# Optimization experiments

Measured on AMD Instinct MI355X. Metric: run time of the kernel, lower is better.

The kernel has to match this reference:

```python
import jax, jax.numpy as jnp
import numpy as np

N_ENVS = 8
MIN_SIGMA = 0.01

def setup_inputs() -> dict:
    key = jax.random.key(0)
    ks = jax.random.split(key, 16)
    B, T, d, L, H = 32, 64, 128, 64, 256
    H2 = H // 2
    s = 0.05
    return {
        "z_signal": jax.random.normal(ks[0], (B, T, d, L), dtype=jnp.float32),
        "z_corrupt": jax.random.normal(ks[1], (B, T, d, L), dtype=jnp.float32),
        "A": jax.random.uniform(ks[2], (d, d), dtype=jnp.float32),
        "regime": jax.random.randint(ks[3], (B,), 0, N_ENVS),
        # signal_proj: Linear(L -> H)
        "W_sig": jax.random.normal(ks[4], (L, H), dtype=jnp.float32) * s,
        "b_sig": jnp.zeros((H,), dtype=jnp.float32),
        # per-env mechanisms: Linear(H->H), ReLU, Linear(H->2), stacked over envs
        "W1e": jax.random.normal(ks[5], (N_ENVS, H, H), dtype=jnp.float32) * s,
        "b1e": jnp.zeros((N_ENVS, H), dtype=jnp.float32),
        "W2e": jax.random.normal(ks[6], (N_ENVS, H, 2), dtype=jnp.float32) * s,
        "b2e": jnp.zeros((N_ENVS, 2), dtype=jnp.float32),
        # corrupt path: Linear(L -> H//2), ReLU, Linear(H//2 -> 1)
        "Wc": jax.random.normal(ks[7], (L, H2), dtype=jnp.float32) * s,
        "bc": jnp.zeros((H2,), dtype=jnp.float32),
        "Wo": jax.random.normal(ks[8], (H2, 1), dtype=jnp.float32) * s,
        "bo": jnp.zeros((1,), dtype=jnp.float32),
    }

def reference(z_signal, z_corrupt, A, regime, W_sig, b_sig, W1e, b1e, W2e, b2e, Wc, bc, Wo, bo):
    # z_signal: [B,T,d,L], A: [d,d]
    # z_agg[b,t,i,l] = sum_j A[j,i] * z_signal[b,t,j,l]  (A^T @ z per slice)
    z_agg = jnp.einsum('ji,btjl->btil', A, z_signal)
    h_signal = jnp.einsum('btdl,lh->btdh', z_agg, W_sig) + b_sig  # [B,T,d,H]

    # env dispatch: e_idx = regime if regime < n_envs else 0 (per batch element)
    eidx = jnp.where(regime >= N_ENVS, 0, regime)
    W1 = W1e[eidx]  # [B,H,H]
    b1 = b1e[eidx]  # [B,H]
    W2 = W2e[eidx]  # [B,H,2]
    b2 = b2e[eidx]  # [B,2]

    h1 = jax.nn.relu(jnp.einsum('btdh,bhk->btdk', h_signal, W1) + b1[:, None, None, :])
    out = jnp.einsum('btdh,bhk->btdk', h1, W2) + b2[:, None, None, :]  # [B,T,d,2]
    mu = out[..., 0]
    sigma = jax.nn.softplus(out[..., 1]) + MIN_SIGMA

    # corrupt contribution
    h_c = jnp.einsum('btdl,lh->btdh', z_corrupt, Wc) + bc
    contrib = (jnp.einsum('btdh,ho->btdo', jax.nn.relu(h_c), Wo) + bo)[..., 0]  # [B,T,d]
    mu = mu + contrib
    return mu, sigma
```

## Files before the change

### kernel.cpp

```cpp
#include <hip/hip_runtime.h>
#include <hip/hip_bf16.h>


typedef __attribute__((ext_vector_type(8))) short short8;
typedef __attribute__((ext_vector_type(4))) float f32x4;

#define MFMA16(a, b, c) __builtin_amdgcn_mfma_f32_16x16x32_bf16((a), (b), (c), 0, 0, 0)

__device__ __forceinline__ unsigned short f2bf(float f) {
  union { float f; unsigned u; } v; v.f = f;
  unsigned r = v.u + 0x7fffu + ((v.u >> 16) & 1u);
  return (unsigned short)(r >> 16);
}

__device__ __forceinline__ unsigned pkbf(float a, float b) {
  __hip_bfloat162 t = __float22bfloat162_rn(float2{a, b});
  unsigned u; __builtin_memcpy(&u, &t, 4); return u;
}

union S8 { short8 s; unsigned u[4]; };

__device__ __forceinline__ void gload16(const void* gsrc, void* ldsdst) {
  __builtin_amdgcn_global_load_lds(
      (const __attribute__((address_space(1))) unsigned int*)gsrc,
      (__attribute__((address_space(3))) unsigned int*)ldsdst, 16, 0, 0);
}

__global__ void setup_k(const float* __restrict__ A, const float* __restrict__ W_sig,
                        const float* __restrict__ b_sig, const float* __restrict__ W1e,
                        const float* __restrict__ b1e, const float* __restrict__ W2e,
                        const float* __restrict__ Wc,
                        unsigned short* __restrict__ wsw1f, unsigned short* __restrict__ at_f,
                        unsigned short* __restrict__ wct_f, float* __restrict__ bw) {
  int blk = blockIdx.x, tid = threadIdx.x;
  if (blk < 512) {
    int e = blk >> 6, l = blk & 63, h = tid;
    const float* w1 = W1e + e * 65536 + h;
    const float* ws = W_sig + l * 256;
    float acc = 0.f;
    #pragma unroll 8
    for (int h1 = 0; h1 < 256; ++h1) acc = fmaf(ws[h1], w1[h1 * 256], acc);
    int c = h >> 7, ht = (h >> 4) & 7, col = h & 15;
    int kks = l >> 5, lgl = (l >> 3) & 3, e8 = l & 7;
    int lane = lgl * 16 + col;
    wsw1f[((((e * 2 + c) * 8 + ht) * 2 + kks) * 64 + lane) * 8 + e8] = f2bf(acc);
  } else if (blk < 576) {
    int idx = (blk - 512) * 256 + tid;
    int frag = idx >> 3, e8 = idx & 7;
    int it = frag >> 8, ks = (frag >> 6) & 3, lane = frag & 63;
    int j = ks * 32 + (lane >> 4) * 8 + e8, i = it * 16 + (lane & 15);
    at_f[idx] = f2bf(A[j * 128 + i]);
  } else if (blk < 608) {
    int idx = (blk - 576) * 256 + tid;
    int frag = idx >> 3, e8 = idx & 7;
    int ht = frag >> 7, ks = (frag >> 6) & 1, lane = frag & 63;
    int l = ks * 32 + (lane >> 4) * 8 + e8, h = ht * 16 + (lane & 15);
    wct_f[idx] = f2bf(Wc[l * 128 + h]);
  } else if (blk < 624) {
    int idx = (blk - 608) * 256 + tid;
    int e = idx >> 9, r = idx & 511;
    bw[e * 768 + 256 + r] = W2e[idx];
  } else {
    int e = blk - 624, h = tid;
    const float* w1 = W1e + e * 65536 + h;
    float acc = b1e[e * 256 + h];
    for (int h1 = 0; h1 < 256; ++h1) acc = fmaf(b_sig[h1], w1[h1 * 256], acc);
    bw[e * 768 + h] = acc;
  }
}

__global__ __launch_bounds__(256, 4) void dec_k(
    const float* __restrict__ zs, const float* __restrict__ zcr,
    const int* __restrict__ regime, const float* __restrict__ b2e,
    const float* __restrict__ bc, const float* __restrict__ Wo,
    const float* __restrict__ bo,
    const unsigned short* __restrict__ wsw1f, const unsigned short* __restrict__ at_f,
    const unsigned short* __restrict__ wct_f, const float* __restrict__ bw,
    float* __restrict__ out) {
  __shared__ __align__(16) char sm[35840];
  float* s_bias1 = (float*)(sm + 32768);
  float* s_W2    = s_bias1 + 256;

  const int bt = ((blockIdx.x & 7) << 8) | (blockIdx.x >> 3);
  const int tid = threadIdx.x;
  const int lane = tid & 63, wave = tid >> 6, lg = lane >> 4, l15 = lane & 15;
  int e = regime[bt >> 6]; if (e >= 8) e = 0;
  const float b2_0 = b2e[2 * e], b2_1 = b2e[2 * e + 1], bo0 = bo[0];

  const float* Z  = zs  + (size_t)bt * 8192;
  const float* Zc = zcr + (size_t)bt * 8192;

  if (wave < 3)
    gload16((const char*)(bw + e * 768) + tid * 16, sm + 32768 + wave * 1024);

  float4 z0v[4], z1v[4];
  #pragma unroll
  for (int k = 0; k < 4; ++k) {
    int g = k * 256 + tid, j = (g >> 4) * 2, l0 = (g & 15) * 4;
    const float* p = Z + j * 64 + l0;
    z0v[k] = *(const float4*)p;
    z1v[k] = *(const float4*)(p + 64);
  }
  float4 zq[2][2][2];
  #pragma unroll
  for (int q = 0; q < 2; ++q) {
    int dcol = (wave * 2 + q) * 16 + l15;
    #pragma unroll
    for (int ks = 0; ks < 2; ++ks) {
      const float* p = Zc + dcol * 64 + ks * 32 + lg * 8;
      zq[q][ks][0] = *(const float4*)p;
      zq[q][ks][1] = *(const float4*)(p + 4);
    }
  }
  #pragma unroll
  for (int k = 0; k < 4; ++k) {
    int g = k * 256 + tid, j = (g >> 4) * 2, l0 = (g & 15) * 4;
    float a0[4] = {z0v[k].x, z0v[k].y, z0v[k].z, z0v[k].w};
    float a1[4] = {z1v[k].x, z1v[k].y, z1v[k].z, z1v[k].w};
    #pragma unroll
    for (int i2 = 0; i2 < 4; ++i2) {
      int l = l0 + i2;
      unsigned v = pkbf(a0[i2], a1[i2]);
      int a = (l * 256 + j * 2) ^ ((((l >> 2) ^ l) & 7) << 4);
      *(unsigned*)(sm + a) = v;
    }
  }
  __syncthreads();

  short8 bq[2][2];
  #pragma unroll
  for (int q = 0; q < 2; ++q)
    #pragma unroll
    for (int ks = 0; ks < 2; ++ks) {
      S8 t;
      t.u[0] = pkbf(zq[q][ks][0].x, zq[q][ks][0].y);
      t.u[1] = pkbf(zq[q][ks][0].z, zq[q][ks][0].w);
      t.u[2] = pkbf(zq[q][ks][1].x, zq[q][ks][1].y);
      t.u[3] = pkbf(zq[q][ks][1].z, zq[q][ks][1].w);
      bq[q][ks] = t.s;
    }

  short8 abfr[2][4];
  #pragma unroll
  for (int m = 0; m < 2; ++m)
    #pragma unroll
    for (int ks = 0; ks < 4; ++ks)
      abfr[m][ks] = *(const short8*)(at_f + ((((wave * 2 + m) * 4 + ks) * 64 + lane) << 3));

  float cp[2] = {0.f, 0.f};
  #pragma unroll
  for (int ht = 0; ht < 8; ++ht) {
    short8 wa0 = *(const short8*)(wct_f + (((ht * 2 + 0) * 64 + lane) << 3));
    short8 wa1 = *(const short8*)(wct_f + (((ht * 2 + 1) * 64 + lane) << 3));
    float4 bcv = *(const float4*)(bc + ht * 16 + lg * 4);
    float4 wov = *(const float4*)(Wo + ht * 16 + lg * 4);
    #pragma unroll
    for (int q = 0; q < 2; ++q) {
      f32x4 acc = (f32x4){0.f, 0.f, 0.f, 0.f};
      acc = MFMA16(wa0, bq[q][0], acc);
      acc = MFMA16(wa1, bq[q][1], acc);
      #pragma unroll
      for (int r = 0; r < 4; ++r)
        cp[q] += fmaxf(acc[r] + bcv[r], 0.f) * wov[r];
    }
  }
  #pragma unroll
  for (int q = 0; q < 2; ++q) {
    cp[q] += __shfl_xor(cp[q], 16);
    cp[q] += __shfl_xor(cp[q], 32);
  }

  const unsigned short* wse = wsw1f + (size_t)e * 16384;
  short8 wsf0[8][2];
  #pragma unroll
  for (int ht = 0; ht < 8; ++ht)
    #pragma unroll
    for (int ks = 0; ks < 2; ++ks)
      wsf0[ht][ks] = *(const short8*)(wse + (((ht * 2 + ks) * 64 + lane) << 3));

  f32x4 acc1[4][2];
  #pragma unroll
  for (int lt = 0; lt < 4; ++lt)
    #pragma unroll
    for (int m = 0; m < 2; ++m) acc1[lt][m] = (f32x4){0.f, 0.f, 0.f, 0.f};
  #pragma unroll
  for (int ks = 0; ks < 4; ++ks) {
    #pragma unroll
    for (int lt = 0; lt < 4; ++lt) {
      int arow = lt * 16 + l15;
      short8 afr = *(const short8*)(sm + ((arow * 256 + lg * 16 + ks * 64) ^
                                          ((((arow >> 2) ^ arow) & 7) << 4)));
      #pragma unroll
      for (int m = 0; m < 2; ++m) acc1[lt][m] = MFMA16(afr, abfr[m][ks], acc1[lt][m]);
    }
  }
  __syncthreads();

  short8 wsf1[8][2];
  #pragma unroll
  for (int ht = 0; ht < 8; ++ht)
    #pragma unroll
    for (int ks = 0; ks < 2; ++ks)
      wsf1[ht][ks] = *(const short8*)(wse + 8192 + (((ht * 2 + ks) * 64 + lane) << 3));

  #pragma unroll
  for (int lt = 0; lt < 4; ++lt) {
    int l0 = lt * 16 + lg * 4;
    #pragma unroll
    for (int m = 0; m < 2; ++m) {
      int i = (wave * 2 + m) * 16 + l15;
      unsigned lo = pkbf(acc1[lt][m][0], acc1[lt][m][1]);
      unsigned hi = pkbf(acc1[lt][m][2], acc1[lt][m][3]);
      int a = (i * 128 + l0 * 2) ^ ((i & 7) << 4);
      *(unsigned long long*)(sm + 16384 + a) = ((unsigned long long)hi << 32) | lo;
    }
  }
  short8 mbfr[2][2];
  #pragma unroll
  for (int m = 0; m < 2; ++m) {
    int brow = (wave * 2 + m) * 16 + l15;
    #pragma unroll
    for (int ks = 0; ks < 2; ++ks)
      mbfr[m][ks] = *(const short8*)(sm + 16384 +
                       ((brow * 128 + lg * 16 + ks * 64) ^ ((brow & 7) << 4)));
  }

  float v0[2] = {0.f, 0.f}, v1[2] = {0.f, 0.f};
  #pragma unroll
  for (int c = 0; c < 2; ++c) {
    #pragma unroll
    for (int ht = 0; ht < 8; ++ht) {
      int h4 = c * 128 + ht * 16 + lg * 4;
      float4 b1v = *(const float4*)(s_bias1 + h4);
      float4 w2a = *(const float4*)(s_W2 + h4 * 2);
      float4 w2b = *(const float4*)(s_W2 + h4 * 2 + 4);
      #pragma unroll
      for (int m = 0; m < 2; ++m) {
        f32x4 acc = (f32x4){0.f, 0.f, 0.f, 0.f};
        if (c == 0) {
          acc = MFMA16(wsf0[ht][0], mbfr[m][0], acc);
          acc = MFMA16(wsf0[ht][1], mbfr[m][1], acc);
        } else {
          acc = MFMA16(wsf1[ht][0], mbfr[m][0], acc);
          acc = MFMA16(wsf1[ht][1], mbfr[m][1], acc);
        }
        float p0 = fmaxf(acc[0] + b1v.x, 0.f), p1 = fmaxf(acc[1] + b1v.y, 0.f);
        float p2 = fmaxf(acc[2] + b1v.z, 0.f), p3 = fmaxf(acc[3] + b1v.w, 0.f);
        v0[m] = fmaf(p0, w2a.x, fmaf(p1, w2a.z, fmaf(p2, w2b.x, fmaf(p3, w2b.z, v0[m]))));
        v1[m] = fmaf(p0, w2a.y, fmaf(p1, w2a.w, fmaf(p2, w2b.y, fmaf(p3, w2b.w, v1[m]))));
      }
    }
  }
  #pragma unroll
  for (int m = 0; m < 2; ++m) {
    v0[m] += __shfl_xor(v0[m], 16); v0[m] += __shfl_xor(v0[m], 32);
    v1[m] += __shfl_xor(v1[m], 16); v1[m] += __shfl_xor(v1[m], 32);
  }

  if (lane < 16) {
    #pragma unroll
    for (int m = 0; m < 2; ++m) {
      int d = (wave * 2 + m) * 16 + lane;
      float mu = v0[m] + b2_0 + bo0 + cp[m];
      float x = v1[m] + b2_1;
      float sg = fmaxf(x, 0.f) + log1pf(expf(-fabsf(x))) + 0.01f;
      out[(size_t)bt * 128 + d] = mu;
      out[262144 + (size_t)bt * 128 + d] = sg;
    }
  }
}

extern "C" void kernel_launch(void* const* d_in, const int* in_sizes, int n_in,
                              void* d_out, int out_size, void* d_ws, size_t ws_size,
                              hipStream_t stream) {
  const float* zs    = (const float*)d_in[0];
  const float* zcr   = (const float*)d_in[1];
  const float* A     = (const float*)d_in[2];
  const int*   reg   = (const int*)d_in[3];
  const float* W_sig = (const float*)d_in[4];
  const float* b_sig = (const float*)d_in[5];
  const float* W1e   = (const float*)d_in[6];
  const float* b1e   = (const float*)d_in[7];
  const float* W2e   = (const float*)d_in[8];
  const float* b2e   = (const float*)d_in[9];
  const float* Wc    = (const float*)d_in[10];
  const float* bcp   = (const float*)d_in[11];
  const float* Wo    = (const float*)d_in[12];
  const float* bo    = (const float*)d_in[13];

  unsigned short* wsw1f = (unsigned short*)d_ws;
  unsigned short* at_f  = wsw1f + 131072;
  unsigned short* wct_f = at_f + 16384;
  float* bw             = (float*)(wct_f + 8192);

  setup_k<<<632, 256, 0, stream>>>(A, W_sig, b_sig, W1e, b1e, W2e, Wc,
                                   wsw1f, at_f, wct_f, bw);
  dec_k<<<2048, 256, 0, stream>>>(zs, zcr, reg, b2e, bcp, Wo, bo,
                                  wsw1f, at_f, wct_f, bw, (float*)d_out);
}
```

Baseline: 52.45 us.

## Process two (b,t) slices per workgroup to reuse weight fragments

Each workgroup now handles two consecutive bt slices instead of one, halving the grid to 1024 blocks. Weight fragments (Wc, W_sig·W1, A) are loaded once into registers and applied to both slices, reducing global/L2 weight traffic per output. In exchange there is more register pressure, an extra barrier, and fewer workgroups for latency hiding. Both slices share the same regime index since bt0 and bt0+1 fall within the same batch.

Measured after the change: 56.51 us. +7.8%, slower.

```diff
diff --git a/kernel.cpp b/kernel.cpp
--- a/kernel.cpp
+++ b/kernel.cpp
@@ -81,63 +81,104 @@
   float* s_bias1 = (float*)(sm + 32768);
   float* s_W2    = s_bias1 + 256;
 
-  const int bt = ((blockIdx.x & 7) << 8) | (blockIdx.x >> 3);
+  const int wg = ((blockIdx.x & 7) << 7) | (blockIdx.x >> 3);
+  const int bt0 = wg * 2;
   const int tid = threadIdx.x;
   const int lane = tid & 63, wave = tid >> 6, lg = lane >> 4, l15 = lane & 15;
-  int e = regime[bt >> 6]; if (e >= 8) e = 0;
+  int e = regime[bt0 >> 6]; if (e >= 8) e = 0;
   const float b2_0 = b2e[2 * e], b2_1 = b2e[2 * e + 1], bo0 = bo[0];
-
-  const float* Z  = zs  + (size_t)bt * 8192;
-  const float* Zc = zcr + (size_t)bt * 8192;
 
   if (wave < 3)
     gload16((const char*)(bw + e * 768) + tid * 16, sm + 32768 + wave * 1024);
 
-  float4 z0v[4], z1v[4];
-  #pragma unroll
-  for (int k = 0; k < 4; ++k) {
-    int g = k * 256 + tid, j = (g >> 4) * 2, l0 = (g & 15) * 4;
-    const float* p = Z + j * 64 + l0;
-    z0v[k] = *(const float4*)p;
-    z1v[k] = *(const float4*)(p + 64);
-  }
-  float4 zq[2][2][2];
-  #pragma unroll
-  for (int q = 0; q < 2; ++q) {
-    int dcol = (wave * 2 + q) * 16 + l15;
-    #pragma unroll
-    for (int ks = 0; ks < 2; ++ks) {
-      const float* p = Zc + dcol * 64 + ks * 32 + lg * 8;
-      zq[q][ks][0] = *(const float4*)p;
-      zq[q][ks][1] = *(const float4*)(p + 4);
-    }
-  }
-  #pragma unroll
-  for (int k = 0; k < 4; ++k) {
-    int g = k * 256 + tid, j = (g >> 4) * 2, l0 = (g & 15) * 4;
-    float a0[4] = {z0v[k].x, z0v[k].y, z0v[k].z, z0v[k].w};
-    float a1[4] = {z1v[k].x, z1v[k].y, z1v[k].z, z1v[k].w};
-    #pragma unroll
-    for (int i2 = 0; i2 < 4; ++i2) {
-      int l = l0 + i2;
-      unsigned v = pkbf(a0[i2], a1[i2]);
-      int a = (l * 256 + j * 2) ^ ((((l >> 2) ^ l) & 7) << 4);
-      *(unsigned*)(sm + a) = v;
+  #pragma unroll
+  for (int g = 0; g < 2; ++g) {
+    const float* Zg = zs + (size_t)(bt0 + g) * 8192;
+    float4 z0v[4], z1v[4];
+    #pragma unroll
+    for (int k = 0; k < 4; ++k) {
+      int gg = k * 256 + tid, j = (gg >> 4) * 2, l0 = (gg & 15) * 4;
+      const float* p = Zg + j * 64 + l0;
+      z0v[k] = *(const float4*)p;
+      z1v[k] = *(const float4*)(p + 64);
+    }
+    #pragma unroll
+    for (int k = 0; k < 4; ++k) {
+      int gg = k * 256 + tid, j = (gg >> 4) * 2, l0 = (gg & 15) * 4;
+      float a0[4] = {z0v[k].x, z0v[k].y, z0v[k].z, z0v[k].w};
+      float a1[4] = {z1v[k].x, z1v[k].y, z1v[k].z, z1v[k].w};
+      #pragma unroll
+      for (int i2 = 0; i2 < 4; ++i2) {
+        int l = l0 + i2;
+        unsigned v = pkbf(a0[i2], a1[i2]);
+        int a = (l * 256 + j * 2) ^ ((((l >> 2) ^ l) & 7) << 4);
+        *(unsigned*)(sm + g * 16384 + a) = v;
+      }
     }
   }
   __syncthreads();
 
-  short8 bq[2][2];
-  #pragma unroll
-  for (int q = 0; q < 2; ++q)
-    #pragma unroll
-    for (int ks = 0; ks < 2; ++ks) {
-      S8 t;
-      t.u[0] = pkbf(zq[q][ks][0].x, zq[q][ks][0].y);
-      t.u[1] = pkbf(zq[q][ks][0].z, zq[q][ks][0].w);
-      t.u[2] = pkbf(zq[q][ks][1].x, zq[q][ks][1].y);
-      t.u[3] = pkbf(zq[q][ks][1].z, zq[q][ks][1].w);
-      bq[q][ks] = t.s;
+  short8 bq[2][2][2];
+  #pragma unroll
+  for (int g = 0; g < 2; ++g) {
+    const float* Zcg = zcr + (size_t)(bt0 + g) * 8192;
+    float4 zq[2][2][2];
+    #pragma unroll
+    for (int q = 0; q < 2; ++q) {
+      int dcol = (wave * 2 + q) * 16 + l15;
+      #pragma unroll
+      for (int ks = 0; ks < 2; ++ks) {
+        const float* p = Zcg + dcol * 64 + ks * 32 + lg * 8;
+        zq[q][ks][0] = *(const float4*)p;
+        zq[q][ks][1] = *(const float4*)(p + 4);
+      }
+    }
+    #pragma unroll
+    for (int q = 0; q < 2; ++q)
+      #pragma unroll
+      for (int ks = 0; ks < 2; ++ks) {
+        S8 t;
+        t.u[0] = pkbf(zq[q][ks][0].x, zq[q][ks][0].y);
+        t.u[1] = pkbf(zq[q][ks][0].z, zq[q][ks][0].w);
+        t.u[2] = pkbf(zq[q][ks][1].x, zq[q][ks][1].y);
+        t.u[3] = pkbf(zq[q][ks][1].z, zq[q][ks][1].w);
+        bq[g][q][ks] = t.s;
+      }
+  }
+
+  float cp[2][2] = {{0.f, 0.f}, {0.f, 0.f}};
+  #pragma unroll
+  for (int hb = 0; hb < 2; ++hb) {
+    short8 wcf[4][2];
+    #pragma unroll
+    for (int hh = 0; hh < 4; ++hh)
+      #pragma unroll
+      for (int ks = 0; ks < 2; ++ks)
+        wcf[hh][ks] = *(const short8*)(wct_f + ((((hb * 4 + hh) * 2 + ks) * 64 + lane) << 3));
+    #pragma unroll
+    for (int hh = 0; hh < 4; ++hh) {
+      int ht = hb * 4 + hh;
+      float4 bcv = *(const float4*)(bc + ht * 16 + lg * 4);
+      float4 wov = *(const float4*)(Wo + ht * 16 + lg * 4);
+      #pragma unroll
+      for (int g = 0; g < 2; ++g)
+        #pragma unroll
+        for (int q = 0; q < 2; ++q) {
+          f32x4 acc = (f32x4){0.f, 0.f, 0.f, 0.f};
+          acc = MFMA16(wcf[hh][0], bq[g][q][0], acc);
+          acc = MFMA16(wcf[hh][1], bq[g][q][1], acc);
+          #pragma unroll
+          for (int r = 0; r < 4; ++r)
+            cp[g][q] += fmaxf(acc[r] + bcv[r], 0.f) * wov[r];
+        }
+    }
+  }
+  #pragma unroll
+  for (int g = 0; g < 2; ++g)
+    #pragma unroll
+    for (int q = 0; q < 2; ++q) {
+      cp[g][q] += __shfl_xor(cp[g][q], 16);
+      cp[g][q] += __shfl_xor(cp[g][q], 32);
     }
 
   short8 abfr[2][4];
@@ -147,126 +188,109 @@
     for (int ks = 0; ks < 4; ++ks)
       abfr[m][ks] = *(const short8*)(at_f + ((((wave * 2 + m) * 4 + ks) * 64 + lane) << 3));
 
-  float cp[2] = {0.f, 0.f};
-  #pragma unroll
-  for (int ht = 0; ht < 8; ++ht) {
-    short8 wa0 = *(const short8*)(wct_f + (((ht * 2 + 0) * 64 + lane) << 3));
-    short8 wa1 = *(const short8*)(wct_f + (((ht * 2 + 1) * 64 + lane) << 3));
-    float4 bcv = *(const float4*)(bc + ht * 16 + lg * 4);
-    float4 wov = *(const float4*)(Wo + ht * 16 + lg * 4);
-    #pragma unroll
-    for (int q = 0; q < 2; ++q) {
-      f32x4 acc = (f32x4){0.f, 0.f, 0.f, 0.f};
-      acc = MFMA16(wa0, bq[q][0], acc);
-      acc = MFMA16(wa1, bq[q][1], acc);
-      #pragma unroll
-      for (int r = 0; r < 4; ++r)
-        cp[q] += fmaxf(acc[r] + bcv[r], 0.f) * wov[r];
-    }
-  }
-  #pragma unroll
-  for (int q = 0; q < 2; ++q) {
-    cp[q] += __shfl_xor(cp[q], 16);
-    cp[q] += __shfl_xor(cp[q], 32);
-  }
-
+  f32x4 acc1[4][2];
+  #pragma unroll
+  for (int g = 0; g < 2; ++g) {
+    #pragma unroll
+    for (int lt = 0; lt < 4; ++lt)
+      #pragma unroll
+      for (int m = 0; m < 2; ++m) acc1[lt][m] = (f32x4){0.f, 0.f, 0.f, 0.f};
+    #pragma unroll
+    for (int ks = 0; ks < 4; ++ks) {
+      #pragma unroll
+      for (int lt = 0; lt < 4; ++lt) {
+        int arow = lt * 16 + l15;
+        short8 afr = *(const short8*)(sm + g * 16384 +
+                        ((arow * 256 + lg * 16 + ks * 64) ^
+                         ((((arow >> 2) ^ arow) & 7) << 4)));
+        acc1[lt][0] = MFMA16(afr, abfr[0][ks], acc1[lt][0]);
+        acc1[lt][1] = MFMA16(afr, abfr[1][ks], acc1[lt][1]);
+      }
+    }
+    __syncthreads();
+    #pragma unroll
+    for (int lt = 0; lt < 4; ++lt) {
+      int l0 = lt * 16 + lg * 4;
+      #pragma unroll
+      for (int m = 0; m < 2; ++m) {
+        int i = (wave * 2 + m) * 16 + l15;
+        unsigned lo = pkbf(acc1[lt][m][0], acc1[lt][m][1]);
+        unsigned hi = pkbf(acc1[lt][m][2], acc1[lt][m][3]);
+        int a = (i * 128 + l0 * 2) ^ ((i & 7) << 4);
+        *(unsigned long long*)(sm + g * 16384 + a) = ((unsigned long long)hi << 32) | lo;
+      }
+    }
+  }
+  __syncthreads();
+
+  short8 mbfr[2][2][2];
+  #pragma unroll
+  for (int g = 0; g < 2; ++g)
+    #pragma unroll
+    for (int m = 0; m < 2; ++m) {
+      int brow = (wave * 2 + m) * 16 + l15;
+      #pragma unroll
+      for (int ks = 0; ks < 2; ++ks)
+        mbfr[g][m][ks] = *(const short8*)(sm + g * 16384 +
+                           ((brow * 128 + lg * 16 + ks * 64) ^ ((brow & 7) << 4)));
+    }
+
+  float v0[2][2] = {{0.f, 0.f}, {0.f, 0.f}}, v1[2][2] = {{0.f, 0.f}, {0.f, 0.f}};
   const unsigned short* wse = wsw1f + (size_t)e * 16384;
-  short8 wsf0[8][2];
-  #pragma unroll
-  for (int ht = 0; ht < 8; ++ht)
-    #pragma unroll
-    for (int ks = 0; ks < 2; ++ks)
-      wsf0[ht][ks] = *(const short8*)(wse + (((ht * 2 + ks) * 64 + lane) << 3));
-
-  f32x4 acc1[4][2];
-  #pragma unroll
-  for (int lt = 0; lt < 4; ++lt)
-    #pragma unroll
-    for (int m = 0; m < 2; ++m) acc1[lt][m] = (f32x4){0.f, 0.f, 0.f, 0.f};
-  #pragma unroll
-  for (int ks = 0; ks < 4; ++ks) {
-    #pragma unroll
-    for (int lt = 0; lt < 4; ++lt) {
-      int arow = lt * 16 + l15;
-      short8 afr = *(const short8*)(sm + ((arow * 256 + lg * 16 + ks * 64) ^
-                                          ((((arow >> 2) ^ arow) & 7) << 4)));
-      #pragma unroll
-      for (int m = 0; m < 2; ++m) acc1[lt][m] = MFMA16(afr, abfr[m][ks], acc1[lt][m]);
-    }
-  }
-  __syncthreads();
-
-  short8 wsf1[8][2];
-  #pragma unroll
-  for (int ht = 0; ht < 8; ++ht)
-    #pragma unroll
-    for (int ks = 0; ks < 2; ++ks)
-      wsf1[ht][ks] = *(const short8*)(wse + 8192 + (((ht * 2 + ks) * 64 + lane) << 3));
-
-  #pragma unroll
-  for (int lt = 0; lt < 4; ++lt) {
-    int l0 = lt * 16 + lg * 4;
+  #pragma unroll
+  for (int c = 0; c < 2; ++c) {
+    #pragma unroll
+    for (int hb = 0; hb < 2; ++hb) {
+      short8 wsf[4][2];
+      #pragma unroll
+      for (int hh = 0; hh < 4; ++hh)
+        #pragma unroll
+        for (int ks = 0; ks < 2; ++ks)
+          wsf[hh][ks] = *(const short8*)(wse +
+                          ((((c * 8 + hb * 4 + hh) * 2 + ks) * 64 + lane) << 3));
+      #pragma unroll
+      for (int hh = 0; hh < 4; ++hh) {
+        int h4 = c * 128 + (hb * 4 + hh) * 16 + lg * 4;
+        float4 b1v = *(const float4*)(s_bias1 + h4);
+        float4 w2a = *(const float4*)(s_W2 + h4 * 2);
+        float4 w2b = *(const float4*)(s_W2 + h4 * 2 + 4);
+        #pragma unroll
+        for (int g = 0; g < 2; ++g)
+          #pragma unroll
+          for (int m = 0; m < 2; ++m) {
+            f32x4 acc = (f32x4){0.f, 0.f, 0.f, 0.f};
+            acc = MFMA16(wsf[hh][0], mbfr[g][m][0], acc);
+            acc = MFMA16(wsf[hh][1], mbfr[g][m][1], acc);
+            float p0 = fmaxf(acc[0] + b1v.x, 0.f), p1 = fmaxf(acc[1] + b1v.y, 0.f);
+            float p2 = fmaxf(acc[2] + b1v.z, 0.f), p3 = fmaxf(acc[3] + b1v.w, 0.f);
+            v0[g][m] = fmaf(p0, w2a.x, fmaf(p1, w2a.z,
+                        fmaf(p2, w2b.x, fmaf(p3, w2b.z, v0[g][m]))));
+            v1[g][m] = fmaf(p0, w2a.y, fmaf(p1, w2a.w,
+                        fmaf(p2, w2b.y, fmaf(p3, w2b.w, v1[g][m]))));
+          }
+      }
+    }
+  }
+  #pragma unroll
+  for (int g = 0; g < 2; ++g)
     #pragma unroll
     for (int m = 0; m < 2; ++m) {
-      int i = (wave * 2 + m) * 16 + l15;
-      unsigned lo = pkbf(acc1[lt][m][0], acc1[lt][m][1]);
-      unsigned hi = pkbf(acc1[lt][m][2], acc1[lt][m][3]);
-      int a = (i * 128 + l0 * 2) ^ ((i & 7) << 4);
-      *(unsigned long long*)(sm + 16384 + a) = ((unsigned long long)hi << 32) | lo;
-    }
-  }
-  short8 mbfr[2][2];
-  #pragma unroll
-  for (int m = 0; m < 2; ++m) {
-    int brow = (wave * 2 + m) * 16 + l15;
-    #pragma unroll
-    for (int ks = 0; ks < 2; ++ks)
-      mbfr[m][ks] = *(const short8*)(sm + 16384 +
-                       ((brow * 128 + lg * 16 + ks * 64) ^ ((brow & 7) << 4)));
-  }
-
-  float v0[2] = {0.f, 0.f}, v1[2] = {0.f, 0.f};
-  #pragma unroll
-  for (int c = 0; c < 2; ++c) {
-    #pragma unroll
-    for (int ht = 0; ht < 8; ++ht) {
-      int h4 = c * 128 + ht * 16 + lg * 4;
-      float4 b1v = *(const float4*)(s_bias1 + h4);
-      float4 w2a = *(const float4*)(s_W2 + h4 * 2);
-      float4 w2b = *(const float4*)(s_W2 + h4 * 2 + 4);
+      v0[g][m] += __shfl_xor(v0[g][m], 16); v0[g][m] += __shfl_xor(v0[g][m], 32);
+      v1[g][m] += __shfl_xor(v1[g][m], 16); v1[g][m] += __shfl_xor(v1[g][m], 32);
+    }
+
+  if (lane < 16) {
+    #pragma unroll
+    for (int g = 0; g < 2; ++g)
       #pragma unroll
       for (int m = 0; m < 2; ++m) {
-        f32x4 acc = (f32x4){0.f, 0.f, 0.f, 0.f};
-        if (c == 0) {
-          acc = MFMA16(wsf0[ht][0], mbfr[m][0], acc);
-          acc = MFMA16(wsf0[ht][1], mbfr[m][1], acc);
-        } else {
-          acc = MFMA16(wsf1[ht][0], mbfr[m][0], acc);
-          acc = MFMA16(wsf1[ht][1], mbfr[m][1], acc);
-        }
-        float p0 = fmaxf(acc[0] + b1v.x, 0.f), p1 = fmaxf(acc[1] + b1v.y, 0.f);
-        float p2 = fmaxf(acc[2] + b1v.z, 0.f), p3 = fmaxf(acc[3] + b1v.w, 0.f);
-        v0[m] = fmaf(p0, w2a.x, fmaf(p1, w2a.z, fmaf(p2, w2b.x, fmaf(p3, w2b.z, v0[m]))));
-        v1[m] = fmaf(p0, w2a.y, fmaf(p1, w2a.w, fmaf(p2, w2b.y, fmaf(p3, w2b.w, v1[m]))));
-      }
-    }
-  }
-  #pragma unroll
-  for (int m = 0; m < 2; ++m) {
-    v0[m] += __shfl_xor(v0[m], 16); v0[m] += __shfl_xor(v0[m], 32);
-    v1[m] += __shfl_xor(v1[m], 16); v1[m] += __shfl_xor(v1[m], 32);
-  }
-
-  if (lane < 16) {
-    #pragma unroll
-    for (int m = 0; m < 2; ++m) {
-      int d = (wave * 2 + m) * 16 + lane;
-      float mu = v0[m] + b2_0 + bo0 + cp[m];
-      float x = v1[m] + b2_1;
-      float sg = fmaxf(x, 0.f) + log1pf(expf(-fabsf(x))) + 0.01f;
-      out[(size_t)bt * 128 + d] = mu;
-      out[262144 + (size_t)bt * 128 + d] = sg;
-    }
+        int d = (wave * 2 + m) * 16 + lane;
+        float mu = v0[g][m] + b2_0 + bo0 + cp[g][m];
+        float x = v1[g][m] + b2_1;
+        float sg = fmaxf(x, 0.f) + log1pf(expf(-fabsf(x))) + 0.01f;
+        out[(size_t)(bt0 + g) * 128 + d] = mu;
+        out[262144 + (size_t)(bt0 + g) * 128 + d] = sg;
+      }
   }
 }
 
@@ -295,6 +319,6 @@
 
   setup_k<<<632, 256, 0, stream>>>(A, W_sig, b_sig, W1e, b1e, W2e, Wc,
                                    wsw1f, at_f, wct_f, bw);
-  dec_k<<<2048, 256, 0, stream>>>(zs, zcr, reg, b2e, bcp, Wo, bo,
+  dec_k<<<1024, 256, 0, stream>>>(zs, zcr, reg, b2e, bcp, Wo, bo,
                                   wsw1f, at_f, wct_f, bw, (float*)d_out);
 }
```
